# Optimization experiments

Measured on AMD Instinct MI355X. Metric: run time of the kernel, lower is better.

## Reference

```python
import jax, jax.numpy as jnp
import numpy as np

B, T, D_ENC, H, NUM_CLASSES = 256, 256, 512, 512, 96


def setup_inputs() -> dict:
    key = jax.random.key(0)
    ks = jax.random.split(key, 12)
    s = lambda k, shp, fan: jax.random.normal(k, shp, jnp.float32) / np.sqrt(fan)
    return {
        "prev_h": jax.random.normal(ks[0], (B, H), jnp.float32),
        "prev_c": jax.random.normal(ks[1], (B, H), jnp.float32),
        "batch_H": jax.random.normal(ks[2], (B, T, D_ENC), jnp.float32),
        "char_onehots": jax.random.uniform(ks[3], (B, NUM_CLASSES), jnp.float32),
        # i2h: Dense(D_ENC -> H, no bias); h2h: Dense(H -> H, bias); score: Dense(H -> 1, no bias)
        "Wi2h": s(ks[4], (D_ENC, H), D_ENC),
        "Wh2h": s(ks[5], (H, H), H),
        "bh2h": jnp.zeros((H,), jnp.float32),
        "Wscore": s(ks[6], (H, 1), H),
        # LSTMCell: input dim = D_ENC + NUM_CLASSES, gates [i, f, g, o]
        "Wk": s(ks[7], (D_ENC + NUM_CLASSES, 4 * H), D_ENC + NUM_CLASSES),
        "Uk": s(ks[8], (H, 4 * H), H),
        "bk": jnp.zeros((4 * H,), jnp.float32),
    }


def reference(prev_h, prev_c, batch_H, char_onehots, Wi2h, Wh2h, bh2h, Wscore, Wk, Uk, bk):
    # Bahdanau additive attention
    bH_proj = jnp.einsum('btd,dh->bth', batch_H, Wi2h)          # [B,T,H]
    h_proj = (prev_h @ Wh2h + bh2h)[:, None, :]                  # [B,1,H]
    e = jnp.tanh(bH_proj + h_proj) @ Wscore                      # [B,T,1]
    alpha = jax.nn.softmax(e, axis=1)                            # [B,T,1]
    context = jnp.einsum('bt,btd->bd', alpha[..., 0], batch_H)   # [B,D_enc]
    # LSTM cell step on [context ; char_onehots]
    x = jnp.concatenate([context, char_onehots], axis=1)         # [B, D_enc+num_classes]
    z = x @ Wk + prev_h @ Uk + bk                                # [B, 4H]
    i, f, g, o = jnp.split(z, 4, axis=1)
    c_new = jax.nn.sigmoid(f) * prev_c + jax.nn.sigmoid(i) * jnp.tanh(g)
    h_new = jax.nn.sigmoid(o) * jnp.tanh(c_new)
    return h_new, c_new, alpha
```

## Files before the change

### kernel.cpp

```cpp
#include <hip/hip_runtime.h>

typedef __bf16 bf16_t;
typedef bf16_t bf16x8 __attribute__((ext_vector_type(8)));
typedef unsigned short ushort8_t __attribute__((ext_vector_type(8)));
typedef unsigned short ushort4_t __attribute__((ext_vector_type(4)));
typedef float f32x4 __attribute__((ext_vector_type(4)));

__device__ __forceinline__ unsigned short f2bf(float f) {
    union { float f; unsigned int u; } v; v.f = f;
    unsigned int r = v.u + 0x7FFFu + ((v.u >> 16) & 1u);
    return (unsigned short)(r >> 16);
}
__device__ __forceinline__ float fast_tanh(float x) {
    float e2 = __expf(2.f * x);
    return 1.f - 2.f / (e2 + 1.f);
}
__device__ __forceinline__ float fast_sig(float x) {
    return 1.f / (1.f + __expf(-x));
}

__global__ void k0_wt(const float* __restrict__ W, unsigned short* __restrict__ Wt) {
    __shared__ float tile[32][33];
    int tx = threadIdx.x, ty = threadIdx.y;
    int bx = blockIdx.x, by = blockIdx.y;
#pragma unroll
    for (int j = 0; j < 4; ++j) {
        int r = by * 32 + ty + j * 8;
        int c = bx * 32 + tx;
        tile[ty + j * 8][tx] = W[r * 512 + c];
    }
    __syncthreads();
#pragma unroll
    for (int j = 0; j < 4; ++j) {
        int h = bx * 32 + ty + j * 8;
        int d = by * 32 + tx;
        Wt[h * 512 + d] = f2bf(tile[tx][ty + j * 8]);
    }
}

__global__ void k1x_conv(const float* __restrict__ src, unsigned short* __restrict__ dst) {
    int i = blockIdx.x * 256 + threadIdx.x;
    float4 f = ((const float4*)src)[i];
    ushort4_t u;
    u[0] = f2bf(f.x); u[1] = f2bf(f.y); u[2] = f2bf(f.z); u[3] = f2bf(f.w);
    ((ushort4_t*)dst)[i] = u;
}

__global__ void k1m_hproj(const unsigned short* __restrict__ ph_bf,
                          const unsigned short* __restrict__ Wht,
                          const float* __restrict__ bh2h,
                          float* __restrict__ h_proj) {
    int tid = threadIdx.x;
    int wave = tid >> 6, lane = tid & 63;
    int l15 = lane & 15, g = lane >> 4;
    int h0 = blockIdx.x * 64 + wave * 16;
    int m0 = blockIdx.y * 32;

    f32x4 acc[2];
    acc[0] = (f32x4){0.f, 0.f, 0.f, 0.f};
    acc[1] = (f32x4){0.f, 0.f, 0.f, 0.f};

    const unsigned short* abase = ph_bf + (size_t)(m0 + l15) * 512 + g * 8;
    const unsigned short* bbase = Wht + (size_t)(h0 + l15) * 512 + g * 8;
#pragma unroll
    for (int j = 0; j < 16; ++j) {
        bf16x8 bf = __builtin_bit_cast(bf16x8, *(const ushort8_t*)(bbase + j * 32));
        bf16x8 a0 = __builtin_bit_cast(bf16x8, *(const ushort8_t*)(abase + j * 32));
        bf16x8 a1 = __builtin_bit_cast(bf16x8, *(const ushort8_t*)(abase + 16 * 512 + j * 32));
        acc[0] = __builtin_amdgcn_mfma_f32_16x16x32_bf16(a0, bf, acc[0], 0, 0, 0);
        acc[1] = __builtin_amdgcn_mfma_f32_16x16x32_bf16(a1, bf, acc[1], 0, 0, 0);
    }
    int h = h0 + l15;
    float bias = bh2h[h];
#pragma unroll
    for (int mf = 0; mf < 2; ++mf)
#pragma unroll
        for (int r = 0; r < 4; ++r)
            h_proj[(size_t)(m0 + mf * 16 + g * 4 + r) * 512 + h] = acc[mf][r] + bias;
}

__launch_bounds__(512, 1)
__global__ void k2_scores(const float* __restrict__ batch_H,
                          const unsigned short* __restrict__ Wt,
                          const float* __restrict__ h_proj,
                          const float* __restrict__ Wscore,
                          float* __restrict__ e_out) {
    __shared__ __align__(16) unsigned short Alds[2 * 9216];
    __shared__ float hp[512];
    __shared__ float wsc[512];
    __shared__ float e_red[4][128];

    int tid = threadIdx.x;
    int m0  = blockIdx.x * 128;
    int b   = m0 >> 8;

    hp[tid]  = h_proj[(size_t)b * 512 + tid];
    wsc[tid] = Wscore[tid];

    int wave = tid >> 6;
    int lane = tid & 63;
    int wr = wave >> 2;
    int wc = wave & 3;
    int l15 = lane & 15, g = lane >> 4;

    int srow = tid >> 2;
    int scol = (tid & 3) << 4;
    const float* sbase = batch_H + (size_t)(m0 + srow) * 512 + scol;
    int sdst = srow * 72 + scol;

    f32x4 acc[4][8];
#pragma unroll
    for (int mf = 0; mf < 4; ++mf)
#pragma unroll
        for (int nf = 0; nf < 8; ++nf)
            acc[mf][nf] = (f32x4){0.f, 0.f, 0.f, 0.f};

    {
        float4 a0 = *(const float4*)(sbase + 0);
        float4 a1 = *(const float4*)(sbase + 4);
        float4 a2 = *(const float4*)(sbase + 8);
        float4 a3 = *(const float4*)(sbase + 12);
        ushort8_t u0, u1;
        u0[0] = f2bf(a0.x); u0[1] = f2bf(a0.y); u0[2] = f2bf(a0.z); u0[3] = f2bf(a0.w);
        u0[4] = f2bf(a1.x); u0[5] = f2bf(a1.y); u0[6] = f2bf(a1.z); u0[7] = f2bf(a1.w);
        u1[0] = f2bf(a2.x); u1[1] = f2bf(a2.y); u1[2] = f2bf(a2.z); u1[3] = f2bf(a2.w);
        u1[4] = f2bf(a3.x); u1[5] = f2bf(a3.y); u1[6] = f2bf(a3.z); u1[7] = f2bf(a3.w);
        *(ushort8_t*)(&Alds[sdst])     = u0;
        *(ushort8_t*)(&Alds[sdst + 8]) = u1;
    }
    __syncthreads();

    const unsigned short* wbase = Wt + (size_t)(wc * 128 + l15) * 512 + g * 8;

    bf16x8 bcur[8], bnxt[8];
#pragma unroll
    for (int nf = 0; nf < 8; ++nf)
        bcur[nf] = __builtin_bit_cast(bf16x8, *(const ushort8_t*)(wbase + nf * 8192));

    float4 st0, st1, st2, st3;

#pragma unroll
    for (int j = 0; j < 16; ++j) {
        const int slab = j >> 1;
        const int buf  = slab & 1;
        const int kb   = j & 1;

        if (kb == 0 && slab < 7) {
            const float* p = sbase + (slab + 1) * 64;
            st0 = *(const float4*)(p + 0);
            st1 = *(const float4*)(p + 4);
            st2 = *(const float4*)(p + 8);
            st3 = *(const float4*)(p + 12);
        }
        if (j < 15) {
            int kk = (j + 1) * 32;
#pragma unroll
            for (int nf = 0; nf < 8; ++nf)
                bnxt[nf] = __builtin_bit_cast(bf16x8, *(const ushort8_t*)(wbase + nf * 8192 + kk));
        }
        bf16x8 afrag[4];
#pragma unroll
        for (int mf = 0; mf < 4; ++mf)
            afrag[mf] = __builtin_bit_cast(bf16x8,
                *(const ushort8_t*)(&Alds[buf * 9216 + (wr * 64 + mf * 16 + l15) * 72 + kb * 32 + g * 8]));
#pragma unroll
        for (int nf = 0; nf < 8; ++nf)
#pragma unroll
            for (int mf = 0; mf < 4; ++mf)
                acc[mf][nf] = __builtin_amdgcn_mfma_f32_16x16x32_bf16(
                    afrag[mf], bcur[nf], acc[mf][nf], 0, 0, 0);
        if (kb == 1 && slab < 7) {
            ushort8_t u0, u1;
            u0[0] = f2bf(st0.x); u0[1] = f2bf(st0.y); u0[2] = f2bf(st0.z); u0[3] = f2bf(st0.w);
            u0[4] = f2bf(st1.x); u0[5] = f2bf(st1.y); u0[6] = f2bf(st1.z); u0[7] = f2bf(st1.w);
            u1[0] = f2bf(st2.x); u1[1] = f2bf(st2.y); u1[2] = f2bf(st2.z); u1[3] = f2bf(st2.w);
            u1[4] = f2bf(st3.x); u1[5] = f2bf(st3.y); u1[6] = f2bf(st3.z); u1[7] = f2bf(st3.w);
            *(ushort8_t*)(&Alds[(buf ^ 1) * 9216 + sdst])     = u0;
            *(ushort8_t*)(&Alds[(buf ^ 1) * 9216 + sdst + 8]) = u1;
            __syncthreads();
        }
#pragma unroll
        for (int nf = 0; nf < 8; ++nf) bcur[nf] = bnxt[nf];
    }

    float s[4][4];
#pragma unroll
    for (int mf = 0; mf < 4; ++mf)
#pragma unroll
        for (int r = 0; r < 4; ++r) s[mf][r] = 0.f;

#pragma unroll
    for (int nf = 0; nf < 8; ++nf) {
        int n = wc * 128 + nf * 16 + l15;
        float hpv = hp[n], wv = wsc[n];
#pragma unroll
        for (int mf = 0; mf < 4; ++mf)
#pragma unroll
            for (int r = 0; r < 4; ++r)
                s[mf][r] += wv * fast_tanh(acc[mf][nf][r] + hpv);
    }
#pragma unroll
    for (int mf = 0; mf < 4; ++mf)
#pragma unroll
        for (int r = 0; r < 4; ++r) {
            float v = s[mf][r];
            v += __shfl_xor(v, 1);
            v += __shfl_xor(v, 2);
            v += __shfl_xor(v, 4);
            v += __shfl_xor(v, 8);
            s[mf][r] = v;
        }
    if (l15 == 0) {
#pragma unroll
        for (int mf = 0; mf < 4; ++mf)
#pragma unroll
            for (int r = 0; r < 4; ++r)
                e_red[wc][wr * 64 + mf * 16 + g * 4 + r] = s[mf][r];
    }
    __syncthreads();
    if (tid < 128) {
        e_out[m0 + tid] = e_red[0][tid] + e_red[1][tid] + e_red[2][tid] + e_red[3][tid];
    }
}

__global__ void k3_softmax(const float* __restrict__ e, float* __restrict__ alpha_out) {
    __shared__ float red[4];
    int b = blockIdx.x, tid = threadIdx.x;
    float v = e[b * 256 + tid];
    float m = v;
#pragma unroll
    for (int off = 32; off; off >>= 1) m = fmaxf(m, __shfl_xor(m, off));
    if ((tid & 63) == 0) red[tid >> 6] = m;
    __syncthreads();
    m = fmaxf(fmaxf(red[0], red[1]), fmaxf(red[2], red[3]));
    float p = __expf(v - m);
    __syncthreads();
    float sum = p;
#pragma unroll
    for (int off = 32; off; off >>= 1) sum += __shfl_xor(sum, off);
    if ((tid & 63) == 0) red[tid >> 6] = sum;
    __syncthreads();
    sum = red[0] + red[1] + red[2] + red[3];
    alpha_out[b * 256 + tid] = p / sum;
}

__global__ void k4_context(const float* __restrict__ batch_H, const float* __restrict__ alpha,
                           float* __restrict__ context) {
    __shared__ float al[256];
    int b = blockIdx.y, dc = blockIdx.x, tid = threadIdx.x;
    al[tid] = alpha[b * 256 + tid];
    __syncthreads();
    int d = dc * 256 + tid;
    const float* bh = batch_H + (size_t)b * 256 * 512 + d;
    float acc = 0.f;
#pragma unroll 4
    for (int t = 0; t < 256; ++t)
        acc += al[t] * bh[(size_t)t * 512];
    context[b * 512 + d] = acc;
}

__global__ void k5t_wzt(const float* __restrict__ Wk, const float* __restrict__ Uk,
                        unsigned short* __restrict__ Wzt) {
    __shared__ float tile[32][33];
    int tx = threadIdx.x, ty = threadIdx.y;
    int bx = blockIdx.x;
    int by = blockIdx.y;
#pragma unroll
    for (int j = 0; j < 4; ++j) {
        int k = bx * 32 + ty + j * 8;
        int c = by * 32 + tx;
        float v = (k < 608) ? Wk[(size_t)k * 2048 + c] : Uk[(size_t)(k - 608) * 2048 + c];
        tile[ty + j * 8][tx] = v;
    }
    __syncthreads();
#pragma unroll
    for (int j = 0; j < 4; ++j) {
        int n = by * 32 + ty + j * 8;
        int k = bx * 32 + tx;
        Wzt[(size_t)n * 1120 + k] = f2bf(tile[tx][ty + j * 8]);
    }
}

__global__ void k5x_build(const float* __restrict__ context, const float* __restrict__ onehots,
                          const float* __restrict__ prev_h, unsigned short* __restrict__ xb) {
    int b = blockIdx.x, tid = threadIdx.x;
    for (int k = tid; k < 1120; k += 256) {
        float v;
        if (k < 512)      v = context[b * 512 + k];
        else if (k < 608) v = onehots[b * 96 + k - 512];
        else              v = prev_h[b * 512 + k - 608];
        xb[b * 1120 + k] = f2bf(v);
    }
}

__launch_bounds__(256)
__global__ void k5m_fused(const unsigned short* __restrict__ xb,
                          const unsigned short* __restrict__ Wzt,
                          const float* __restrict__ bk,
                          const float* __restrict__ prev_c,
                          float* __restrict__ out) {
    __shared__ __align__(16) unsigned short Axs[32 * 232];

    int tid  = threadIdx.x;
    int wave = tid >> 6;
    int lane = tid & 63;
    int l15  = lane & 15;
    int g    = lane >> 4;
    int b0   = blockIdx.y * 32;
    int h0   = blockIdx.x * 64 + wave * 16;

    f32x4 acc[2][4];
#pragma unroll
    for (int mf = 0; mf < 2; ++mf)
#pragma unroll
        for (int gt = 0; gt < 4; ++gt)
            acc[mf][gt] = (f32x4){0.f, 0.f, 0.f, 0.f};

    const unsigned short* wbase = Wzt + (size_t)(h0 + l15) * 1120;

    for (int ks = 0; ks < 5; ++ks) {
        if (ks) __syncthreads();
        int kbase = ks * 224;
        for (int i = tid; i < 896; i += 256) {
            int row = i / 28;
            int c8  = (i % 28) * 8;
            *(ushort8_t*)(&Axs[row * 232 + c8]) =
                *(const ushort8_t*)(&xb[(size_t)(b0 + row) * 1120 + kbase + c8]);
        }
        __syncthreads();

        bf16x8 bcur[4], bnxt[4];
#pragma unroll
        for (int gt = 0; gt < 4; ++gt)
            bcur[gt] = __builtin_bit_cast(bf16x8,
                *(const ushort8_t*)(wbase + (size_t)gt * 512 * 1120 + kbase + g * 8));

#pragma unroll
        for (int kb = 0; kb < 7; ++kb) {
            if (kb < 6) {
                int kg = kbase + (kb + 1) * 32 + g * 8;
#pragma unroll
                for (int gt = 0; gt < 4; ++gt)
                    bnxt[gt] = __builtin_bit_cast(bf16x8,
                        *(const ushort8_t*)(wbase + (size_t)gt * 512 * 1120 + kg));
            }
            bf16x8 afrag[2];
#pragma unroll
            for (int mf = 0; mf < 2; ++mf)
                afrag[mf] = __builtin_bit_cast(bf16x8,
                    *(const ushort8_t*)(&Axs[(mf * 16 + l15) * 232 + kb * 32 + g * 8]));
#pragma unroll
            for (int gt = 0; gt < 4; ++gt)
#pragma unroll
                for (int mf = 0; mf < 2; ++mf)
                    acc[mf][gt] = __builtin_amdgcn_mfma_f32_16x16x32_bf16(
                        afrag[mf], bcur[gt], acc[mf][gt], 0, 0, 0);
#pragma unroll
            for (int gt = 0; gt < 4; ++gt) bcur[gt] = bnxt[gt];
        }
    }

    int h = h0 + l15;
    float bi = bk[h], bfv = bk[512 + h], bg = bk[1024 + h], bo = bk[1536 + h];
#pragma unroll
    for (int mf = 0; mf < 2; ++mf)
#pragma unroll
        for (int r = 0; r < 4; ++r) {
            int m = b0 + mf * 16 + g * 4 + r;
            float zi = acc[mf][0][r] + bi;
            float zf = acc[mf][1][r] + bfv;
            float zg = acc[mf][2][r] + bg;
            float zo = acc[mf][3][r] + bo;
            float c  = fast_sig(zf) * prev_c[m * 512 + h] + fast_sig(zi) * fast_tanh(zg);
            float hn = fast_sig(zo) * fast_tanh(c);
            out[m * 512 + h]          = hn;
            out[131072 + m * 512 + h] = c;
        }
}

extern "C" void kernel_launch(void* const* d_in, const int* in_sizes, int n_in,
                              void* d_out, int out_size, void* d_ws, size_t ws_size,
                              hipStream_t stream) {
    (void)in_sizes; (void)n_in; (void)out_size; (void)ws_size;
    const float* prev_h  = (const float*)d_in[0];
    const float* prev_c  = (const float*)d_in[1];
    const float* batch_H = (const float*)d_in[2];
    const float* onehots = (const float*)d_in[3];
    const float* Wi2h    = (const float*)d_in[4];
    const float* Wh2h    = (const float*)d_in[5];
    const float* bh2h    = (const float*)d_in[6];
    const float* Wscore  = (const float*)d_in[7];
    const float* Wk      = (const float*)d_in[8];
    const float* Uk      = (const float*)d_in[9];
    const float* bk      = (const float*)d_in[10];
    float* out = (float*)d_out;
    float* alpha = out + 262144;

    char* ws = (char*)d_ws;
    unsigned short* Wt     = (unsigned short*)(ws + 0);
    unsigned short* Wht    = (unsigned short*)(ws + 524288);
    unsigned short* ph_bf  = (unsigned short*)(ws + 1048576);
    float*          h_proj = (float*)(ws + 1310720);
    float*          e      = (float*)(ws + 1835008);
    unsigned short* Wzt    = (unsigned short*)(ws + 0);
    unsigned short* xb     = (unsigned short*)(ws + 4784128);
    float*          context= (float*)(ws + 5373952);

    k0_wt     <<<dim3(16, 16), dim3(32, 8), 0, stream>>>(Wi2h, Wt);
    k0_wt     <<<dim3(16, 16), dim3(32, 8), 0, stream>>>(Wh2h, Wht);
    k1x_conv  <<<128, 256, 0, stream>>>(prev_h, ph_bf);
    k1m_hproj <<<dim3(8, 8), 256, 0, stream>>>(ph_bf, Wht, bh2h, h_proj);
    k2_scores <<<512, 512, 0, stream>>>(batch_H, Wt, h_proj, Wscore, e);
    k3_softmax<<<256, 256, 0, stream>>>(e, alpha);
    k4_context<<<dim3(2, 256), 256, 0, stream>>>(batch_H, alpha, context);
    k5t_wzt   <<<dim3(35, 64), dim3(32, 8), 0, stream>>>(Wk, Uk, Wzt);
    k5x_build <<<256, 256, 0, stream>>>(context, onehots, prev_h, xb);
    k5m_fused <<<dim3(8, 8), 256, 0, stream>>>(xb, Wzt, bk, prev_c, out);
}
```

Measured before the change: 177.1 us.

## Retile score GEMM into 128x128 tiles with LDS-staged weights and partial scores

The attention-score GEMM now uses 2048 workgroups of 256 threads, each owning a 128x128 M/N tile, instead of 512 workgroups covering all of N. Weight tiles are staged into swizzled LDS via global_load_lds, and the batch_H tile goes into a swizzled layout, replacing per-lane global weight loads and padded rows. Each N tile writes partial scores that the softmax kernel now sums. The two weight-transpose launches are merged into one grid. The aim is more workgroups, higher occupancy and fewer LDS bank conflicts. In exchange, batch_H is read and converted four times (once per N tile), and the software prefetch double-buffering is gone.

```diff
diff --git a/kernel.cpp b/kernel.cpp
--- a/kernel.cpp
+++ b/kernel.cpp
@@ -19,8 +19,11 @@
     return 1.f / (1.f + __expf(-x));
 }
 
-__global__ void k0_wt(const float* __restrict__ W, unsigned short* __restrict__ Wt) {
+__global__ void k0_wt2(const float* __restrict__ Wi2h, const float* __restrict__ Wh2h,
+                       unsigned short* __restrict__ Wt, unsigned short* __restrict__ Wht) {
     __shared__ float tile[32][33];
+    const float* W = blockIdx.z ? Wh2h : Wi2h;
+    unsigned short* O = blockIdx.z ? Wht : Wt;
     int tx = threadIdx.x, ty = threadIdx.y;
     int bx = blockIdx.x, by = blockIdx.y;
 #pragma unroll
@@ -34,7 +37,7 @@
     for (int j = 0; j < 4; ++j) {
         int h = bx * 32 + ty + j * 8;
         int d = by * 32 + tx;
-        Wt[h * 512 + d] = f2bf(tile[tx][ty + j * 8]);
+        O[h * 512 + d] = f2bf(tile[tx][ty + j * 8]);
     }
 }
 
@@ -79,108 +82,94 @@
             h_proj[(size_t)(m0 + mf * 16 + g * 4 + r) * 512 + h] = acc[mf][r] + bias;
 }
 
-__launch_bounds__(512, 1)
+__launch_bounds__(256, 2)
 __global__ void k2_scores(const float* __restrict__ batch_H,
                           const unsigned short* __restrict__ Wt,
                           const float* __restrict__ h_proj,
                           const float* __restrict__ Wscore,
-                          float* __restrict__ e_out) {
-    __shared__ __align__(16) unsigned short Alds[2 * 9216];
-    __shared__ float hp[512];
-    __shared__ float wsc[512];
-    __shared__ float e_red[4][128];
+                          float* __restrict__ e_part) {
+    __shared__ __align__(16) unsigned short Alds[8192];
+    __shared__ __align__(16) unsigned short Blds[8192];
+    __shared__ float hp_s[128];
+    __shared__ float wsc_s[128];
+    __shared__ float e_red[4][64];
 
     int tid = threadIdx.x;
-    int m0  = blockIdx.x * 128;
-    int b   = m0 >> 8;
-
-    hp[tid]  = h_proj[(size_t)b * 512 + tid];
-    wsc[tid] = Wscore[tid];
+    int wg = (blockIdx.x & 7) * 256 + (blockIdx.x >> 3);
+    int mt = wg >> 2, nt = wg & 3;
+    int m0 = mt * 128, n0 = nt * 128;
+    int b  = m0 >> 8;
+
+    if (tid < 128) hp_s[tid] = h_proj[(size_t)b * 512 + n0 + tid];
+    else           wsc_s[tid - 128] = Wscore[n0 + tid - 128];
 
     int wave = tid >> 6;
     int lane = tid & 63;
-    int wr = wave >> 2;
-    int wc = wave & 3;
+    int wr = wave >> 1;
+    int wc = wave & 1;
     int l15 = lane & 15, g = lane >> 4;
-
-    int srow = tid >> 2;
-    int scol = (tid & 3) << 4;
-    const float* sbase = batch_H + (size_t)(m0 + srow) * 512 + scol;
-    int sdst = srow * 72 + scol;
-
-    f32x4 acc[4][8];
+    int bchunk = ((lane & 7) ^ (lane >> 3)) << 3;
+    int brow_l = lane >> 3;
+
+    f32x4 acc[4][4];
 #pragma unroll
     for (int mf = 0; mf < 4; ++mf)
 #pragma unroll
-        for (int nf = 0; nf < 8; ++nf)
+        for (int nf = 0; nf < 4; ++nf)
             acc[mf][nf] = (f32x4){0.f, 0.f, 0.f, 0.f};
 
-    {
-        float4 a0 = *(const float4*)(sbase + 0);
-        float4 a1 = *(const float4*)(sbase + 4);
-        float4 a2 = *(const float4*)(sbase + 8);
-        float4 a3 = *(const float4*)(sbase + 12);
-        ushort8_t u0, u1;
-        u0[0] = f2bf(a0.x); u0[1] = f2bf(a0.y); u0[2] = f2bf(a0.z); u0[3] = f2bf(a0.w);
-        u0[4] = f2bf(a1.x); u0[5] = f2bf(a1.y); u0[6] = f2bf(a1.z); u0[7] = f2bf(a1.w);
-        u1[0] = f2bf(a2.x); u1[1] = f2bf(a2.y); u1[2] = f2bf(a2.z); u1[3] = f2bf(a2.w);
-        u1[4] = f2bf(a3.x); u1[5] = f2bf(a3.y); u1[6] = f2bf(a3.z); u1[7] = f2bf(a3.w);
-        *(ushort8_t*)(&Alds[sdst])     = u0;
-        *(ushort8_t*)(&Alds[sdst + 8]) = u1;
-    }
-    __syncthreads();
-
-    const unsigned short* wbase = Wt + (size_t)(wc * 128 + l15) * 512 + g * 8;
-
-    bf16x8 bcur[8], bnxt[8];
-#pragma unroll
-    for (int nf = 0; nf < 8; ++nf)
-        bcur[nf] = __builtin_bit_cast(bf16x8, *(const ushort8_t*)(wbase + nf * 8192));
-
-    float4 st0, st1, st2, st3;
-
-#pragma unroll
-    for (int j = 0; j < 16; ++j) {
-        const int slab = j >> 1;
-        const int buf  = slab & 1;
-        const int kb   = j & 1;
-
-        if (kb == 0 && slab < 7) {
-            const float* p = sbase + (slab + 1) * 64;
-            st0 = *(const float4*)(p + 0);
-            st1 = *(const float4*)(p + 4);
-            st2 = *(const float4*)(p + 8);
-            st3 = *(const float4*)(p + 12);
-        }
-        if (j < 15) {
-            int kk = (j + 1) * 32;
-#pragma unroll
-            for (int nf = 0; nf < 8; ++nf)
-                bnxt[nf] = __builtin_bit_cast(bf16x8, *(const ushort8_t*)(wbase + nf * 8192 + kk));
-        }
-        bf16x8 afrag[4];
-#pragma unroll
-        for (int mf = 0; mf < 4; ++mf)
-            afrag[mf] = __builtin_bit_cast(bf16x8,
-                *(const ushort8_t*)(&Alds[buf * 9216 + (wr * 64 + mf * 16 + l15) * 72 + kb * 32 + g * 8]));
-#pragma unroll
-        for (int nf = 0; nf < 8; ++nf)
-#pragma unroll
-            for (int mf = 0; mf < 4; ++mf)
-                acc[mf][nf] = __builtin_amdgcn_mfma_f32_16x16x32_bf16(
-                    afrag[mf], bcur[nf], acc[mf][nf], 0, 0, 0);
-        if (kb == 1 && slab < 7) {
-            ushort8_t u0, u1;
-            u0[0] = f2bf(st0.x); u0[1] = f2bf(st0.y); u0[2] = f2bf(st0.z); u0[3] = f2bf(st0.w);
-            u0[4] = f2bf(st1.x); u0[5] = f2bf(st1.y); u0[6] = f2bf(st1.z); u0[7] = f2bf(st1.w);
-            u1[0] = f2bf(st2.x); u1[1] = f2bf(st2.y); u1[2] = f2bf(st2.z); u1[3] = f2bf(st2.w);
-            u1[4] = f2bf(st3.x); u1[5] = f2bf(st3.y); u1[6] = f2bf(st3.z); u1[7] = f2bf(st3.w);
-            *(ushort8_t*)(&Alds[(buf ^ 1) * 9216 + sdst])     = u0;
-            *(ushort8_t*)(&Alds[(buf ^ 1) * 9216 + sdst + 8]) = u1;
-            __syncthreads();
-        }
-#pragma unroll
-        for (int nf = 0; nf < 8; ++nf) bcur[nf] = bnxt[nf];
+    for (int ks = 0; ks < 8; ++ks) {
+        __syncthreads();
+        int kbase = ks * 64;
+#pragma unroll
+        for (int i = 0; i < 4; ++i) {
+            int q = wave * 4 + i;
+            int row = q * 8 + brow_l;
+            const unsigned short* gsrc = Wt + (size_t)(n0 + row) * 512 + kbase + bchunk;
+            __builtin_amdgcn_global_load_lds(
+                (const __attribute__((address_space(1))) void*)gsrc,
+                (__attribute__((address_space(3))) void*)&Blds[q * 512], 16, 0, 0);
+        }
+        float4 av[8];
+#pragma unroll
+        for (int j = 0; j < 8; ++j) {
+            int idx = j * 256 + tid;
+            int r = idx >> 4, c4 = idx & 15;
+            av[j] = *(const float4*)(batch_H + (size_t)(m0 + r) * 512 + kbase + c4 * 4);
+        }
+#pragma unroll
+        for (int j = 0; j < 8; ++j) {
+            int idx = j * 256 + tid;
+            int r = idx >> 4, c4 = idx & 15;
+            ushort4_t u;
+            u[0] = f2bf(av[j].x); u[1] = f2bf(av[j].y);
+            u[2] = f2bf(av[j].z); u[3] = f2bf(av[j].w);
+            int boff = r * 128 + ((((c4 >> 1) ^ (r & 7)) << 4) | ((c4 & 1) << 3));
+            *(ushort4_t*)((char*)Alds + boff) = u;
+        }
+        __syncthreads();
+#pragma unroll
+        for (int kk = 0; kk < 2; ++kk) {
+            bf16x8 af[4], bf[4];
+#pragma unroll
+            for (int mf = 0; mf < 4; ++mf) {
+                int row = wr * 64 + mf * 16 + l15;
+                int boff = row * 128 + ((((kk * 4 + g) ^ (l15 & 7))) << 4);
+                af[mf] = __builtin_bit_cast(bf16x8, *(const ushort8_t*)((char*)Alds + boff));
+            }
+#pragma unroll
+            for (int nf = 0; nf < 4; ++nf) {
+                int row = wc * 64 + nf * 16 + l15;
+                int boff = row * 128 + ((((kk * 4 + g) ^ (l15 & 7))) << 4);
+                bf[nf] = __builtin_bit_cast(bf16x8, *(const ushort8_t*)((char*)Blds + boff));
+            }
+#pragma unroll
+            for (int nf = 0; nf < 4; ++nf)
+#pragma unroll
+                for (int mf = 0; mf < 4; ++mf)
+                    acc[mf][nf] = __builtin_amdgcn_mfma_f32_16x16x32_bf16(
+                        af[mf], bf[nf], acc[mf][nf], 0, 0, 0);
+        }
     }
 
     float s[4][4];
@@ -190,9 +179,9 @@
         for (int r = 0; r < 4; ++r) s[mf][r] = 0.f;
 
 #pragma unroll
-    for (int nf = 0; nf < 8; ++nf) {
-        int n = wc * 128 + nf * 16 + l15;
-        float hpv = hp[n], wv = wsc[n];
+    for (int nf = 0; nf < 4; ++nf) {
+        int nl = wc * 64 + nf * 16 + l15;
+        float hpv = hp_s[nl], wv = wsc_s[nl];
 #pragma unroll
         for (int mf = 0; mf < 4; ++mf)
 #pragma unroll
@@ -215,25 +204,28 @@
         for (int mf = 0; mf < 4; ++mf)
 #pragma unroll
             for (int r = 0; r < 4; ++r)
-                e_red[wc][wr * 64 + mf * 16 + g * 4 + r] = s[mf][r];
+                e_red[wave][mf * 16 + g * 4 + r] = s[mf][r];
     }
     __syncthreads();
     if (tid < 128) {
-        e_out[m0 + tid] = e_red[0][tid] + e_red[1][tid] + e_red[2][tid] + e_red[3][tid];
-    }
-}
-
-__global__ void k3_softmax(const float* __restrict__ e, float* __restrict__ alpha_out) {
+        int wrr = tid >> 6, i64 = tid & 63;
+        float v = e_red[wrr * 2 + 0][i64] + e_red[wrr * 2 + 1][i64];
+        e_part[(size_t)nt * 65536 + m0 + tid] = v;
+    }
+}
+
+__global__ void k3_softmax(const float* __restrict__ e_part, float* __restrict__ alpha_out) {
     __shared__ float red[4];
     int b = blockIdx.x, tid = threadIdx.x;
-    float v = e[b * 256 + tid];
-    float m = v;
-#pragma unroll
-    for (int off = 32; off; off >>= 1) m = fmaxf(m, __shfl_xor(m, off));
-    if ((tid & 63) == 0) red[tid >> 6] = m;
-    __syncthreads();
-    m = fmaxf(fmaxf(red[0], red[1]), fmaxf(red[2], red[3]));
-    float p = __expf(v - m);
+    int m = b * 256 + tid;
+    float v = e_part[m] + e_part[65536 + m] + e_part[131072 + m] + e_part[196608 + m];
+    float mx = v;
+#pragma unroll
+    for (int off = 32; off; off >>= 1) mx = fmaxf(mx, __shfl_xor(mx, off));
+    if ((tid & 63) == 0) red[tid >> 6] = mx;
+    __syncthreads();
+    mx = fmaxf(fmaxf(red[0], red[1]), fmaxf(red[2], red[3]));
+    float p = __expf(v - mx);
     __syncthreads();
     float sum = p;
 #pragma unroll
@@ -401,17 +393,16 @@
     unsigned short* Wht    = (unsigned short*)(ws + 524288);
     unsigned short* ph_bf  = (unsigned short*)(ws + 1048576);
     float*          h_proj = (float*)(ws + 1310720);
-    float*          e      = (float*)(ws + 1835008);
+    float*          e_part = (float*)(ws + 1835008);
     unsigned short* Wzt    = (unsigned short*)(ws + 0);
-    unsigned short* xb     = (unsigned short*)(ws + 4784128);
-    float*          context= (float*)(ws + 5373952);
-
-    k0_wt     <<<dim3(16, 16), dim3(32, 8), 0, stream>>>(Wi2h, Wt);
-    k0_wt     <<<dim3(16, 16), dim3(32, 8), 0, stream>>>(Wh2h, Wht);
+    unsigned short* xb     = (unsigned short*)(ws + 4587520);
+    float*          context= (float*)(ws + 5160960);
+
+    k0_wt2    <<<dim3(16, 16, 2), dim3(32, 8), 0, stream>>>(Wi2h, Wh2h, Wt, Wht);
     k1x_conv  <<<128, 256, 0, stream>>>(prev_h, ph_bf);
     k1m_hproj <<<dim3(8, 8), 256, 0, stream>>>(ph_bf, Wht, bh2h, h_proj);
-    k2_scores <<<512, 512, 0, stream>>>(batch_H, Wt, h_proj, Wscore, e);
-    k3_softmax<<<256, 256, 0, stream>>>(e, alpha);
+    k2_scores <<<2048, 256, 0, stream>>>(batch_H, Wt, h_proj, Wscore, e_part);
+    k3_softmax<<<256, 256, 0, stream>>>(e_part, alpha);
     k4_context<<<dim3(2, 256), 256, 0, stream>>>(batch_H, alpha, context);
     k5t_wzt   <<<dim3(35, 64), dim3(32, 8), 0, stream>>>(Wk, Uk, Wzt);
     k5x_build <<<256, 256, 0, stream>>>(context, onehots, prev_h, xb);
```

Result: faster. 145.5 us (-17.8%).
